# Kernel optimization log

Hardware: AMD Instinct MI355X
Metric: run time of the kernel (lower is better)

Reference implementation:

```python
import jax, jax.numpy as jnp
import numpy as np

N = 50000        # num nodes
E = 800000       # num edges (no self loops by construction)
D = 128          # in_features == out_features
NE = 4           # num_envs
EPS = 1e-8
STDV = 1.0 / np.sqrt(D)


def setup_inputs() -> dict:
    key = jax.random.key(0)
    k = jax.random.split(key, 6)
    x = jax.random.normal(k[0], (N, D), jnp.float32)
    row = jax.random.randint(k[1], (E,), 0, N, dtype=jnp.int32)
    off = jax.random.randint(k[2], (E,), 1, N, dtype=jnp.int32)
    col = (row + off) % N  # guarantees no self loops (matches remove_self_loops)
    adj = jnp.stack([row, col])
    env_weights = jax.random.uniform(k[3], (N, NE), jnp.float32)
    weights = jax.random.uniform(k[4], (NE, D, D), jnp.float32, -STDV, STDV)
    a = jax.random.normal(k[5], (NE, 2 * D, 1), jnp.float32) * np.sqrt(2.0 / (2 * D + 1)) * 1.414
    return {"x": x, "adj": adj, "env_weights": env_weights, "weights": weights, "a": a}


def reference(x, adj, env_weights, weights, a):
    n = x.shape[0]
    f = weights.shape[-1]
    loops = jnp.arange(n, dtype=adj.dtype)
    src = jnp.concatenate([adj[0], loops])  # add_self_loops
    dst = jnp.concatenate([adj[1], loops])
    # per-env projected features: [NE, N, F]
    h = jnp.einsum('nd,edf->enf', x, weights)
    # attention logits: cat(h[src], h[dst]) @ a  ==  h[src]@a1 + h[dst]@a2
    a1 = a[:, :f, 0]   # [NE, F]
    a2 = a[:, f:, 0]   # [NE, F]
    s_src = jnp.einsum('enf,ef->en', h, a1)
    s_dst = jnp.einsum('enf,ef->en', h, a2)
    logits = jax.nn.leaky_relu(s_src[:, src] + s_dst[:, dst], 0.01)  # [NE, Etot]
    # global per-env max subtraction (as in the torch code: max over all edges)
    e = jnp.exp(logits - jnp.max(logits, axis=1, keepdims=True))
    def agg(ek, hk):
        # specialspmm: out[src] += ek * hk[dst]; denom via ones vector
        denom = jax.ops.segment_sum(ek, src, num_segments=n) + EPS          # [N]
        num = jax.ops.segment_sum(ek[:, None] * hk[dst], src, num_segments=n)  # [N, F]
        return num / denom[:, None]
    out_env = jax.vmap(agg)(e, h)  # [NE, N, F]
    out = jnp.einsum('ne,enf->nf', env_weights, out_env)
    return out + x  # residual
```

## Files before the change

kernel.cpp:

```cpp
#include <hip/hip_runtime.h>

#define N_NODES 50000
#define N_EDGES 800000
#define D_FEAT  128
#define NE_ENV  4
#define EPS_F   1e-8f
#define M_CONST 4.0f
#define SCAN_NB 196
#define NB_BUCKET 391
#define BINA_EPT 16

typedef __attribute__((ext_vector_type(8))) short bf16x8;
typedef __attribute__((ext_vector_type(4))) float floatx4;
typedef __attribute__((ext_vector_type(2))) float f32x2;

static __device__ __forceinline__ unsigned short f2bf(float v) {
    union { float f; unsigned int u; } c; c.f = v;
    unsigned int u = c.u;
    u += 0x7fffu + ((u >> 16) & 1u);
    return (unsigned short)(u >> 16);
}

static __device__ __forceinline__ f32x2 bf2f(unsigned int v) {
    f32x2 r;
    r.x = __uint_as_float(v << 16);
    r.y = __uint_as_float(v & 0xffff0000u);
    return r;
}

static __device__ __forceinline__ float lrelu_exp(float z) {
    float lk = z > 0.f ? z : 0.01f * z;
    return __expf(lk - M_CONST);
}

static __device__ __forceinline__ void pk_add(f32x2& acc, f32x2 w) {
    asm("v_pk_add_f32 %0, %1, %0" : "+v"(acc) : "v"(w));
}
static __device__ __forceinline__ void pk_fma_bl(f32x2& acc, f32x2 w, f32x2 x) {
    asm("v_pk_fma_f32 %0, %1, %2, %0 op_sel:[0,0,0] op_sel_hi:[0,1,1]" : "+v"(acc) : "v"(w), "v"(x));
}
static __device__ __forceinline__ void pk_fma_bh(f32x2& acc, f32x2 w, f32x2 x) {
    asm("v_pk_fma_f32 %0, %1, %2, %0 op_sel:[1,0,0] op_sel_hi:[1,1,1]" : "+v"(acc) : "v"(w), "v"(x));
}

static __device__ __forceinline__ void edge_acc(unsigned int xv, float4 w,
        f32x2& den01, f32x2& den23, f32x2* axy) {
    f32x2 x = bf2f(xv);
    f32x2 wxy; wxy.x = w.x; wxy.y = w.y;
    f32x2 wzw; wzw.x = w.z; wzw.y = w.w;
    pk_add(den01, wxy);
    pk_add(den23, wzw);
    pk_fma_bl(axy[0], wxy, x);
    pk_fma_bh(axy[1], wxy, x);
    pk_fma_bl(axy[2], wzw, x);
    pk_fma_bh(axy[3], wzw, x);
}

__global__ __launch_bounds__(256) void k_setup(const float* __restrict__ weights, const float* __restrict__ a,
        float* __restrict__ b, unsigned short* __restrict__ wsw,
        const int* __restrict__ row, int* __restrict__ counts) {
    int blk = blockIdx.x;
    if (blk < 128) {
        int wave = threadIdx.x >> 6, lane = threadIdx.x & 63;
        int t = blk * 4 + wave;
        int e = t >> 7, d = t & 127;
        float2 w2 = ((const float2*)(weights + e * 16384 + d * 128))[lane];
        float2 a1 = ((const float2*)(a + e * 256))[lane];
        float2 a2 = ((const float2*)(a + e * 256 + 128))[lane];
        float p1 = w2.x * a1.x + w2.y * a1.y;
        float p2 = w2.x * a2.x + w2.y * a2.y;
#pragma unroll
        for (int off = 32; off > 0; off >>= 1) {
            p1 += __shfl_xor(p1, off, 64);
            p2 += __shfl_xor(p2, off, 64);
        }
        if (lane == 0) {
            b[e * 128 + d] = p1;
            b[512 + e * 128 + d] = p2;
        }
    } else if (blk < 384) {
        int idx = (blk - 128) * 256 + threadIdx.x;
        int j = idx & 7;
        int l = (idx >> 3) & 63;
        int t = (idx >> 9) & 7;
        int s = idx >> 12;
        int k = s * 32 + (l >> 4) * 8 + j;
        int f = t * 16 + (l & 15);
        int e = k >> 7, d = k & 127;
        wsw[idx] = f2bf(weights[e * 16384 + d * 128 + f]);
    } else {
        int k = (blk - 384) * 256 + threadIdx.x;
        if (k < N_EDGES) atomicAdd(&counts[row[k]], 1);
    }
}

__global__ __launch_bounds__(256) void k_s(const float* __restrict__ x, const float* __restrict__ b,
        float* __restrict__ s_src, float* __restrict__ s_dst, unsigned short* __restrict__ xbf) {
    int wave = threadIdx.x >> 6, lane = threadIdx.x & 63;
    int gw = blockIdx.x * 4 + wave;
    if (gw >= 3125) return;
    int quad = lane >> 4, lm = lane & 15;
    int base = gw * 16;

    floatx4 acc = (floatx4){0.f, 0.f, 0.f, 0.f};
    const float* xrow = x + (size_t)(base + lm) * 128 + quad * 8;
    unsigned short* xbrow = xbf + (size_t)(base + lm) * 128 + quad * 8;

#pragma unroll
    for (int s = 0; s < 4; ++s) {
        float4 lo = *(const float4*)(xrow + s * 32);
        float4 hi = *(const float4*)(xrow + s * 32 + 4);
        bf16x8 af;
        af[0] = (short)f2bf(lo.x); af[1] = (short)f2bf(lo.y);
        af[2] = (short)f2bf(lo.z); af[3] = (short)f2bf(lo.w);
        af[4] = (short)f2bf(hi.x); af[5] = (short)f2bf(hi.y);
        af[6] = (short)f2bf(hi.z); af[7] = (short)f2bf(hi.w);
        *(bf16x8*)(xbrow + s * 32) = af;

        bf16x8 bfv = (bf16x8){0, 0, 0, 0, 0, 0, 0, 0};
        if (lm < 8) {
            const float* bp = b + lm * 128 + s * 32 + quad * 8;
            float4 b0 = *(const float4*)bp;
            float4 b1 = *(const float4*)(bp + 4);
            bfv[0] = (short)f2bf(b0.x); bfv[1] = (short)f2bf(b0.y);
            bfv[2] = (short)f2bf(b0.z); bfv[3] = (short)f2bf(b0.w);
            bfv[4] = (short)f2bf(b1.x); bfv[5] = (short)f2bf(b1.y);
            bfv[6] = (short)f2bf(b1.z); bfv[7] = (short)f2bf(b1.w);
        }
        acc = __builtin_amdgcn_mfma_f32_16x16x32_bf16(af, bfv, acc, 0, 0, 0);
    }
    if (lm < 8) {
        float* dstp = (lm < 4) ? (s_src + (size_t)(base + quad * 4) * 4 + lm)
                               : (s_dst + (size_t)(base + quad * 4) * 4 + (lm - 4));
#pragma unroll
        for (int r = 0; r < 4; ++r) dstp[r * 4] = acc[r];
    }
}

__global__ void k_scan_a(const int* __restrict__ counts, int* __restrict__ partial) {
    __shared__ int sm[256];
    int idx = blockIdx.x * 256 + threadIdx.x;
    sm[threadIdx.x] = (idx < N_NODES) ? counts[idx] : 0;
    __syncthreads();
    for (int s = 128; s > 0; s >>= 1) {
        if (threadIdx.x < s) sm[threadIdx.x] += sm[threadIdx.x + s];
        __syncthreads();
    }
    if (threadIdx.x == 0) partial[blockIdx.x] = sm[0];
}

__global__ void k_scan_b(const int* __restrict__ partial, int* __restrict__ chunk_off) {
    __shared__ int sm[256];
    int t = threadIdx.x;
    int v = (t < SCAN_NB) ? partial[t] : 0;
    sm[t] = v;
    __syncthreads();
    for (int s2 = 1; s2 < 256; s2 <<= 1) {
        int add = (t >= s2) ? sm[t - s2] : 0;
        __syncthreads();
        sm[t] += add;
        __syncthreads();
    }
    chunk_off[t] = sm[t] - v;
}

__global__ void k_scan_c(const int* __restrict__ counts, const int* __restrict__ chunk_off,
                         int* __restrict__ offsets, int* __restrict__ bcur) {
    __shared__ int sm[256];
    int t = threadIdx.x;
    int idx = blockIdx.x * 256 + t;
    int v = (idx < N_NODES) ? counts[idx] : 0;
    sm[t] = v;
    __syncthreads();
    for (int s2 = 1; s2 < 256; s2 <<= 1) {
        int add = (t >= s2) ? sm[t - s2] : 0;
        __syncthreads();
        sm[t] += add;
        __syncthreads();
    }
    if (idx < N_NODES) {
        int excl = chunk_off[blockIdx.x] + sm[t] - v;
        offsets[idx] = excl;
        if ((idx & 127) == 0) bcur[idx >> 7] = excl;
    }
    if (idx == 0) offsets[N_NODES] = N_EDGES;
}

__global__ __launch_bounds__(256) void k_binA(const int* __restrict__ row, const int* __restrict__ col,
        int* __restrict__ bcur, unsigned int* __restrict__ binned) {
    __shared__ int cnt[NB_BUCKET];
    __shared__ int base[NB_BUCKET];
    int t = threadIdx.x;
    for (int b = t; b < NB_BUCKET; b += 256) cnt[b] = 0;
    __syncthreads();
    unsigned int pk[BINA_EPT];
    int ebase = blockIdx.x * (256 * BINA_EPT) + t;
#pragma unroll
    for (int j = 0; j < BINA_EPT; ++j) {
        int k = ebase + j * 256;
        pk[j] = 0xffffffffu;
        if (k < N_EDGES) {
            unsigned int s = (unsigned int)row[k];
            unsigned int d = (unsigned int)col[k];
            pk[j] = (s << 16) | d;
            atomicAdd(&cnt[s >> 7], 1);
        }
    }
    __syncthreads();
    for (int b = t; b < NB_BUCKET; b += 256) {
        int c = cnt[b];
        base[b] = c ? atomicAdd(&bcur[b], c) : 0;
        cnt[b] = 0;
    }
    __syncthreads();
#pragma unroll
    for (int j = 0; j < BINA_EPT; ++j) {
        if (pk[j] != 0xffffffffu) {
            int b = pk[j] >> 23;
            int off = atomicAdd(&cnt[b], 1);
            binned[base[b] + off] = pk[j];
        }
    }
}

__global__ __launch_bounds__(256) void k_binB(const unsigned int* __restrict__ binned,
        const int* __restrict__ offsets,
        const float* __restrict__ s_src, const float* __restrict__ s_dst,
        int* __restrict__ sorted_dst, float4* __restrict__ w_sorted) {
    __shared__ int cur[128];
    int b = blockIdx.x;
    int nb = b << 7;
    int nc = min(128, N_NODES - nb);
    int t = threadIdx.x;
    if (t < nc) cur[t] = offsets[nb + t];
    __syncthreads();
    int ebeg = offsets[nb];
    int eend = offsets[nb + nc];
    for (int i = ebeg + t; i < eend; i += 256) {
        unsigned int pk = binned[i];
        int s = (int)(pk >> 16), d = (int)(pk & 0xffffu);
        float4 a4 = *(const float4*)(s_src + s * 4);
        float4 b4 = *(const float4*)(s_dst + d * 4);
        float4 w;
        w.x = lrelu_exp(a4.x + b4.x);
        w.y = lrelu_exp(a4.y + b4.y);
        w.z = lrelu_exp(a4.z + b4.z);
        w.w = lrelu_exp(a4.w + b4.w);
        int pos = atomicAdd(&cur[s - nb], 1);
        sorted_dst[pos] = d;
        w_sorted[pos] = w;
    }
}

__global__ __launch_bounds__(256) void k_agg_gemm(const unsigned int* __restrict__ xb,
        const float* __restrict__ s_src, const float* __restrict__ s_dst,
        const int* __restrict__ offsets, const int* __restrict__ sorted_dst,
        const float4* __restrict__ w_sorted, const float* __restrict__ env_w,
        const unsigned short* __restrict__ Wsw,
        const float* __restrict__ x, float* __restrict__ out) {
    __shared__ __align__(16) unsigned int Gsm[16 * 256];
    int wave = threadIdx.x >> 6, lane = threadIdx.x & 63;
    int nb = blockIdx.x * 16;

#pragma unroll 1
    for (int j = 0; j < 4; ++j) {
        int r = wave * 4 + j;
        int n = nb + r;

        f32x2 den01, den23;
        f32x2 axy[4];
        {
            float4 sa = *(const float4*)(s_src + n * 4);
            float4 sb = *(const float4*)(s_dst + n * 4);
            float ws0 = lrelu_exp(sa.x + sb.x), ws1 = lrelu_exp(sa.y + sb.y);
            float ws2 = lrelu_exp(sa.z + sb.z), ws3 = lrelu_exp(sa.w + sb.w);
            f32x2 xv = bf2f(xb[((unsigned)n << 6) + lane]);
            den01.x = ws0; den01.y = ws1;
            den23.x = ws2; den23.y = ws3;
            axy[0].x = ws0 * xv.x; axy[0].y = ws0 * xv.y;
            axy[1].x = ws1 * xv.x; axy[1].y = ws1 * xv.y;
            axy[2].x = ws2 * xv.x; axy[2].y = ws2 * xv.y;
            axy[3].x = ws3 * xv.x; axy[3].y = ws3 * xv.y;
        }

        int beg = __builtin_amdgcn_readfirstlane(offsets[n]);
        int end = __builtin_amdgcn_readfirstlane(offsets[n + 1]);
        int i = beg;
        for (; i + 7 < end; i += 8) {
            int d[8]; float4 w[8]; unsigned int v[8];
#pragma unroll
            for (int q = 0; q < 8; ++q) d[q] = sorted_dst[i + q];
#pragma unroll
            for (int q = 0; q < 8; ++q) v[q] = xb[((unsigned)d[q] << 6) + lane];
#pragma unroll
            for (int q = 0; q < 8; ++q) w[q] = w_sorted[i + q];
#pragma unroll
            for (int q = 0; q < 8; ++q) edge_acc(v[q], w[q], den01, den23, axy);
        }
        for (; i + 3 < end; i += 4) {
            int d[4]; float4 w[4]; unsigned int v[4];
#pragma unroll
            for (int q = 0; q < 4; ++q) d[q] = sorted_dst[i + q];
#pragma unroll
            for (int q = 0; q < 4; ++q) v[q] = xb[((unsigned)d[q] << 6) + lane];
#pragma unroll
            for (int q = 0; q < 4; ++q) w[q] = w_sorted[i + q];
#pragma unroll
            for (int q = 0; q < 4; ++q) edge_acc(v[q], w[q], den01, den23, axy);
        }
        for (; i < end; ++i) {
            int d0 = sorted_dst[i];
            edge_acc(xb[((unsigned)d0 << 6) + lane], w_sorted[i], den01, den23, axy);
        }

        float4 ewt = *(const float4*)(env_w + n * 4);
        float ewv[4] = { ewt.x, ewt.y, ewt.z, ewt.w };
        float dens[4] = { den01.x, den01.y, den23.x, den23.y };
        int swz = (r & 7) << 2;
#pragma unroll
        for (int e = 0; e < 4; ++e) {
            float sc = ewv[e] / (dens[e] + EPS_F);
            unsigned int lo = f2bf(sc * axy[e].x);
            unsigned int hi = f2bf(sc * axy[e].y);
            Gsm[(r * 256 + e * 64 + lane) ^ swz] = (hi << 16) | lo;
        }
    }
    __syncthreads();

    int quad = lane >> 4, lm = lane & 15;
    int t0 = wave * 2;
    floatx4 acc0 = (floatx4){0.f, 0.f, 0.f, 0.f};
    floatx4 acc1 = (floatx4){0.f, 0.f, 0.f, 0.f};
    int rswz = (lm & 7) << 2;
#pragma unroll
    for (int s = 0; s < 16; ++s) {
        int idx = (lm * 256 + s * 16 + quad * 4) ^ rswz;
        bf16x8 af = *(const bf16x8*)(&Gsm[idx]);
        bf16x8 b0 = *(const bf16x8*)(Wsw + (((s * 8 + t0) * 64 + lane) * 8));
        bf16x8 b1 = *(const bf16x8*)(Wsw + (((s * 8 + t0 + 1) * 64 + lane) * 8));
        acc0 = __builtin_amdgcn_mfma_f32_16x16x32_bf16(af, b0, acc0, 0, 0, 0);
        acc1 = __builtin_amdgcn_mfma_f32_16x16x32_bf16(af, b1, acc1, 0, 0, 0);
    }
    int row_base = nb + quad * 4;
#pragma unroll
    for (int r = 0; r < 4; ++r) {
        int rowi = row_base + r;
        int c0 = t0 * 16 + lm;
        int c1 = c0 + 16;
        out[rowi * 128 + c0] = acc0[r] + x[rowi * 128 + c0];
        out[rowi * 128 + c1] = acc1[r] + x[rowi * 128 + c1];
    }
}

extern "C" void kernel_launch(void* const* d_in, const int* in_sizes, int n_in,
                              void* d_out, int out_size, void* d_ws, size_t ws_size,
                              hipStream_t stream) {
    const float* x       = (const float*)d_in[0];
    const int*   adj     = (const int*)d_in[1];
    const int*   row     = adj;
    const int*   col     = adj + N_EDGES;
    const float* env_w   = (const float*)d_in[2];
    const float* weights = (const float*)d_in[3];
    const float* a       = (const float*)d_in[4];
    float* out = (float*)d_out;

    char* ws = (char*)d_ws;
    size_t off = 0;
    auto alloc = [&](size_t bytes) -> char* {
        char* p = ws + off;
        off += (bytes + 255) & ~(size_t)255;
        return p;
    };
    float* b          = (float*)alloc(1024 * 4);
    float* s_src      = (float*)alloc((size_t)N_NODES * 4 * 4);
    float* s_dst      = (float*)alloc((size_t)N_NODES * 4 * 4);
    int*   counts     = (int*)alloc((size_t)N_NODES * 4);
    int*   offsets    = (int*)alloc((size_t)(N_NODES + 1) * 4);
    int*   partial    = (int*)alloc(256 * 4);
    int*   chunk_off  = (int*)alloc(256 * 4);
    int*   bcur       = (int*)alloc(512 * 4);
    unsigned int* binned = (unsigned int*)alloc((size_t)N_EDGES * 4);
    int*   sorted_dst = (int*)alloc((size_t)N_EDGES * 4);
    float4* w_sorted  = (float4*)alloc((size_t)N_EDGES * 16);
    unsigned short* wsw = (unsigned short*)alloc(65536 * 2);
    unsigned short* xbf = (unsigned short*)alloc((size_t)N_NODES * 128 * 2);

    hipMemsetAsync(counts, 0, (size_t)N_NODES * 4, stream);
    k_setup<<<3509, 256, 0, stream>>>(weights, a, b, wsw, row, counts);
    k_s<<<782, 256, 0, stream>>>(x, b, s_src, s_dst, xbf);
    k_scan_a<<<SCAN_NB, 256, 0, stream>>>(counts, partial);
    k_scan_b<<<1, 256, 0, stream>>>(partial, chunk_off);
    k_scan_c<<<SCAN_NB, 256, 0, stream>>>(counts, chunk_off, offsets, bcur);
    k_binA<<<196, 256, 0, stream>>>(row, col, bcur, binned);
    k_binB<<<NB_BUCKET, 256, 0, stream>>>(binned, offsets, s_src, s_dst, sorted_dst, w_sorted);
    k_agg_gemm<<<3125, 256, 0, stream>>>((const unsigned int*)xbf, s_src, s_dst, offsets,
                                         sorted_dst, w_sorted, env_w, wsw, x, out);
}
```

Baseline: 213.5 us.

## Replace per-node count scan with bucket histogram and enlarge aggregation GEMM blocks

Edge counting now builds per-bucket histograms in shared memory instead of doing per-node global atomics. A single small kernel scans the 391 bucket counts, replacing the three-kernel node scan, and the per-node offsets are produced inside k_binB from a local histogram. Separately, the aggregation+GEMM kernel moves to 512-thread blocks covering 32 nodes. Each wave keeps its 16 weight fragments in registers and reuses them across two row tiles. This removes 800K global atomics and two launches, at the cost of more register pressure and a masked tail block.

```diff
diff --git a/kernel.cpp b/kernel.cpp
--- a/kernel.cpp
+++ b/kernel.cpp
@@ -6,9 +6,10 @@
 #define NE_ENV  4
 #define EPS_F   1e-8f
 #define M_CONST 4.0f
-#define SCAN_NB 196
 #define NB_BUCKET 391
 #define BINA_EPT 16
+#define NBH 200
+#define EH  4000
 
 typedef __attribute__((ext_vector_type(8))) short bf16x8;
 typedef __attribute__((ext_vector_type(4))) float floatx4;
@@ -58,7 +59,7 @@
 
 __global__ __launch_bounds__(256) void k_setup(const float* __restrict__ weights, const float* __restrict__ a,
         float* __restrict__ b, unsigned short* __restrict__ wsw,
-        const int* __restrict__ row, int* __restrict__ counts) {
+        const int* __restrict__ row, int* __restrict__ bcnt) {
     int blk = blockIdx.x;
     if (blk < 128) {
         int wave = threadIdx.x >> 6, lane = threadIdx.x & 63;
@@ -89,8 +90,20 @@
         int e = k >> 7, d = k & 127;
         wsw[idx] = f2bf(weights[e * 16384 + d * 128 + f]);
     } else {
-        int k = (blk - 384) * 256 + threadIdx.x;
-        if (k < N_EDGES) atomicAdd(&counts[row[k]], 1);
+        __shared__ int h[NB_BUCKET];
+        int t = threadIdx.x;
+        for (int i = t; i < NB_BUCKET; i += 256) h[i] = 0;
+        __syncthreads();
+        int e0 = (blk - 384) * EH;
+        for (int j = t; j < EH; j += 256) {
+            int k = e0 + j;
+            if (k < N_EDGES) atomicAdd(&h[row[k] >> 7], 1);
+        }
+        __syncthreads();
+        for (int i = t; i < NB_BUCKET; i += 256) {
+            int c = h[i];
+            if (c) atomicAdd(&bcnt[i], c);
+        }
     }
 }
 
@@ -137,53 +150,23 @@
     }
 }
 
-__global__ void k_scan_a(const int* __restrict__ counts, int* __restrict__ partial) {
-    __shared__ int sm[256];
-    int idx = blockIdx.x * 256 + threadIdx.x;
-    sm[threadIdx.x] = (idx < N_NODES) ? counts[idx] : 0;
-    __syncthreads();
-    for (int s = 128; s > 0; s >>= 1) {
-        if (threadIdx.x < s) sm[threadIdx.x] += sm[threadIdx.x + s];
-        __syncthreads();
-    }
-    if (threadIdx.x == 0) partial[blockIdx.x] = sm[0];
-}
-
-__global__ void k_scan_b(const int* __restrict__ partial, int* __restrict__ chunk_off) {
-    __shared__ int sm[256];
+__global__ void k_bscan(const int* __restrict__ bcnt, int* __restrict__ bbase,
+                        int* __restrict__ bcur, int* __restrict__ offsets) {
+    __shared__ int sm[512];
     int t = threadIdx.x;
-    int v = (t < SCAN_NB) ? partial[t] : 0;
+    int v = (t < NB_BUCKET) ? bcnt[t] : 0;
     sm[t] = v;
     __syncthreads();
-    for (int s2 = 1; s2 < 256; s2 <<= 1) {
+    for (int s2 = 1; s2 < 512; s2 <<= 1) {
         int add = (t >= s2) ? sm[t - s2] : 0;
         __syncthreads();
         sm[t] += add;
         __syncthreads();
     }
-    chunk_off[t] = sm[t] - v;
-}
-
-__global__ void k_scan_c(const int* __restrict__ counts, const int* __restrict__ chunk_off,
-                         int* __restrict__ offsets, int* __restrict__ bcur) {
-    __shared__ int sm[256];
-    int t = threadIdx.x;
-    int idx = blockIdx.x * 256 + t;
-    int v = (idx < N_NODES) ? counts[idx] : 0;
-    sm[t] = v;
-    __syncthreads();
-    for (int s2 = 1; s2 < 256; s2 <<= 1) {
-        int add = (t >= s2) ? sm[t - s2] : 0;
-        __syncthreads();
-        sm[t] += add;
-        __syncthreads();
-    }
-    if (idx < N_NODES) {
-        int excl = chunk_off[blockIdx.x] + sm[t] - v;
-        offsets[idx] = excl;
-        if ((idx & 127) == 0) bcur[idx >> 7] = excl;
-    }
-    if (idx == 0) offsets[N_NODES] = N_EDGES;
+    int excl = sm[t] - v;
+    if (t < NB_BUCKET) { bbase[t] = excl; bcur[t] = excl; }
+    if (t == NB_BUCKET) bbase[t] = excl;
+    if (t == 0) offsets[N_NODES] = N_EDGES;
 }
 
 __global__ __launch_bounds__(256) void k_binA(const int* __restrict__ row, const int* __restrict__ col,
@@ -224,18 +207,35 @@
 }
 
 __global__ __launch_bounds__(256) void k_binB(const unsigned int* __restrict__ binned,
-        const int* __restrict__ offsets,
+        const int* __restrict__ bbase,
         const float* __restrict__ s_src, const float* __restrict__ s_dst,
-        int* __restrict__ sorted_dst, float4* __restrict__ w_sorted) {
+        int* __restrict__ offsets, int* __restrict__ sorted_dst, float4* __restrict__ w_sorted) {
+    __shared__ int hist[128];
     __shared__ int cur[128];
     int b = blockIdx.x;
     int nb = b << 7;
     int nc = min(128, N_NODES - nb);
     int t = threadIdx.x;
-    if (t < nc) cur[t] = offsets[nb + t];
-    __syncthreads();
-    int ebeg = offsets[nb];
-    int eend = offsets[nb + nc];
+    if (t < 128) hist[t] = 0;
+    __syncthreads();
+    int ebeg = bbase[b];
+    int eend = bbase[b + 1];
+    for (int i = ebeg + t; i < eend; i += 256)
+        atomicAdd(&hist[(binned[i] >> 16) & 127], 1);
+    __syncthreads();
+    int v = (t < 128) ? hist[t] : 0;
+    for (int s2 = 1; s2 < 128; s2 <<= 1) {
+        int add = (t >= s2 && t < 128) ? hist[t - s2] : 0;
+        __syncthreads();
+        if (t < 128) hist[t] += add;
+        __syncthreads();
+    }
+    if (t < 128) {
+        int pos = ebeg + hist[t] - v;
+        cur[t] = pos;
+        if (t < nc) offsets[nb + t] = pos;
+    }
+    __syncthreads();
     for (int i = ebeg + t; i < eend; i += 256) {
         unsigned int pk = binned[i];
         int s = (int)(pk >> 16), d = (int)(pk & 0xffffu);
@@ -246,26 +246,32 @@
         w.y = lrelu_exp(a4.y + b4.y);
         w.z = lrelu_exp(a4.z + b4.z);
         w.w = lrelu_exp(a4.w + b4.w);
-        int pos = atomicAdd(&cur[s - nb], 1);
+        int pos = atomicAdd(&cur[s & 127], 1);
         sorted_dst[pos] = d;
         w_sorted[pos] = w;
     }
 }
 
-__global__ __launch_bounds__(256) void k_agg_gemm(const unsigned int* __restrict__ xb,
+__global__ __launch_bounds__(512) void k_agg_gemm(const unsigned int* __restrict__ xb,
         const float* __restrict__ s_src, const float* __restrict__ s_dst,
         const int* __restrict__ offsets, const int* __restrict__ sorted_dst,
         const float4* __restrict__ w_sorted, const float* __restrict__ env_w,
         const unsigned short* __restrict__ Wsw,
         const float* __restrict__ x, float* __restrict__ out) {
-    __shared__ __align__(16) unsigned int Gsm[16 * 256];
+    __shared__ __align__(16) unsigned int Gsm[32 * 256];
     int wave = threadIdx.x >> 6, lane = threadIdx.x & 63;
-    int nb = blockIdx.x * 16;
+    int nb = blockIdx.x * 32;
 
 #pragma unroll 1
     for (int j = 0; j < 4; ++j) {
         int r = wave * 4 + j;
         int n = nb + r;
+        int swz = (r & 7) << 2;
+        if (n >= N_NODES) {
+#pragma unroll
+            for (int e = 0; e < 4; ++e) Gsm[(r * 256 + e * 64 + lane) ^ swz] = 0;
+            continue;
+        }
 
         f32x2 den01, den23;
         f32x2 axy[4];
@@ -316,7 +322,6 @@
         float4 ewt = *(const float4*)(env_w + n * 4);
         float ewv[4] = { ewt.x, ewt.y, ewt.z, ewt.w };
         float dens[4] = { den01.x, den01.y, den23.x, den23.y };
-        int swz = (r & 7) << 2;
 #pragma unroll
         for (int e = 0; e < 4; ++e) {
             float sc = ewv[e] / (dens[e] + EPS_F);
@@ -328,27 +333,28 @@
     __syncthreads();
 
     int quad = lane >> 4, lm = lane & 15;
-    int t0 = wave * 2;
-    floatx4 acc0 = (floatx4){0.f, 0.f, 0.f, 0.f};
-    floatx4 acc1 = (floatx4){0.f, 0.f, 0.f, 0.f};
+    int cb = wave;
+    bf16x8 Bf[16];
+#pragma unroll
+    for (int s = 0; s < 16; ++s)
+        Bf[s] = *(const bf16x8*)(Wsw + (((s * 8 + cb) * 64 + lane) * 8));
     int rswz = (lm & 7) << 2;
 #pragma unroll
-    for (int s = 0; s < 16; ++s) {
-        int idx = (lm * 256 + s * 16 + quad * 4) ^ rswz;
-        bf16x8 af = *(const bf16x8*)(&Gsm[idx]);
-        bf16x8 b0 = *(const bf16x8*)(Wsw + (((s * 8 + t0) * 64 + lane) * 8));
-        bf16x8 b1 = *(const bf16x8*)(Wsw + (((s * 8 + t0 + 1) * 64 + lane) * 8));
-        acc0 = __builtin_amdgcn_mfma_f32_16x16x32_bf16(af, b0, acc0, 0, 0, 0);
-        acc1 = __builtin_amdgcn_mfma_f32_16x16x32_bf16(af, b1, acc1, 0, 0, 0);
-    }
-    int row_base = nb + quad * 4;
-#pragma unroll
-    for (int r = 0; r < 4; ++r) {
-        int rowi = row_base + r;
-        int c0 = t0 * 16 + lm;
-        int c1 = c0 + 16;
-        out[rowi * 128 + c0] = acc0[r] + x[rowi * 128 + c0];
-        out[rowi * 128 + c1] = acc1[r] + x[rowi * 128 + c1];
+    for (int rt = 0; rt < 2; ++rt) {
+        floatx4 acc = (floatx4){0.f, 0.f, 0.f, 0.f};
+#pragma unroll
+        for (int s = 0; s < 16; ++s) {
+            int idx = (((rt * 16 + lm) * 256 + s * 16 + quad * 4) ^ rswz);
+            bf16x8 af = *(const bf16x8*)(&Gsm[idx]);
+            acc = __builtin_amdgcn_mfma_f32_16x16x32_bf16(af, Bf[s], acc, 0, 0, 0);
+        }
+        int row_base = nb + rt * 16 + quad * 4;
+        int c = cb * 16 + lm;
+#pragma unroll
+        for (int r = 0; r < 4; ++r) {
+            int rowi = row_base + r;
+            if (rowi < N_NODES) out[rowi * 128 + c] = acc[r] + x[rowi * 128 + c];
+        }
     }
 }
 
@@ -374,10 +380,9 @@
     float* b          = (float*)alloc(1024 * 4);
     float* s_src      = (float*)alloc((size_t)N_NODES * 4 * 4);
     float* s_dst      = (float*)alloc((size_t)N_NODES * 4 * 4);
-    int*   counts     = (int*)alloc((size_t)N_NODES * 4);
     int*   offsets    = (int*)alloc((size_t)(N_NODES + 1) * 4);
-    int*   partial    = (int*)alloc(256 * 4);
-    int*   chunk_off  = (int*)alloc(256 * 4);
+    int*   bcnt       = (int*)alloc(512 * 4);
+    int*   bbase      = (int*)alloc(512 * 4);
     int*   bcur       = (int*)alloc(512 * 4);
     unsigned int* binned = (unsigned int*)alloc((size_t)N_EDGES * 4);
     int*   sorted_dst = (int*)alloc((size_t)N_EDGES * 4);
@@ -385,14 +390,12 @@
     unsigned short* wsw = (unsigned short*)alloc(65536 * 2);
     unsigned short* xbf = (unsigned short*)alloc((size_t)N_NODES * 128 * 2);
 
-    hipMemsetAsync(counts, 0, (size_t)N_NODES * 4, stream);
-    k_setup<<<3509, 256, 0, stream>>>(weights, a, b, wsw, row, counts);
+    hipMemsetAsync(bcnt, 0, 512 * 4, stream);
+    k_setup<<<384 + NBH, 256, 0, stream>>>(weights, a, b, wsw, row, bcnt);
     k_s<<<782, 256, 0, stream>>>(x, b, s_src, s_dst, xbf);
-    k_scan_a<<<SCAN_NB, 256, 0, stream>>>(counts, partial);
-    k_scan_b<<<1, 256, 0, stream>>>(partial, chunk_off);
-    k_scan_c<<<SCAN_NB, 256, 0, stream>>>(counts, chunk_off, offsets, bcur);
+    k_bscan<<<1, 512, 0, stream>>>(bcnt, bbase, bcur, offsets);
     k_binA<<<196, 256, 0, stream>>>(row, col, bcur, binned);
-    k_binB<<<NB_BUCKET, 256, 0, stream>>>(binned, offsets, s_src, s_dst, sorted_dst, w_sorted);
-    k_agg_gemm<<<3125, 256, 0, stream>>>((const unsigned int*)xbf, s_src, s_dst, offsets,
+    k_binB<<<NB_BUCKET, 256, 0, stream>>>(binned, bbase, s_src, s_dst, offsets, sorted_dst, w_sorted);
+    k_agg_gemm<<<1563, 512, 0, stream>>>((const unsigned int*)xbf, s_src, s_dst, offsets,
                                          sorted_dst, w_sorted, env_w, wsw, x, out);
 }
```

After: 208.1 us. -2.5%, faster.
